# Kernel tuning notes

Hardware: AMD Instinct MI355X
Metric: run time of the kernel (lower is better)

The kernel has to match this reference:

```python
import jax, jax.numpy as jnp
import numpy as np

B, S, D, H = 2, 4096, 512, 8
HD = D // H  # 64


def setup_inputs() -> dict:
    key = jax.random.key(0)
    ks = jax.random.split(key, 9)
    def lin_init(kw, kb, fan_in, fan_out):
        bound = 1.0 / np.sqrt(fan_in)
        W = jax.random.uniform(kw, (fan_in, fan_out), minval=-bound, maxval=bound, dtype=jnp.float32)
        b = jax.random.uniform(kb, (fan_out,), minval=-bound, maxval=bound, dtype=jnp.float32)
        return W, b
    Wq, bq = lin_init(ks[0], ks[1], D, D)
    Wk, bk = lin_init(ks[2], ks[3], D, D)
    Wv, bv = lin_init(ks[4], ks[5], D, D)
    query = jax.random.normal(ks[6], (B, S, D), dtype=jnp.float32)
    key_in = jax.random.normal(ks[7], (B, S, D), dtype=jnp.float32)
    value = jax.random.normal(ks[8], (B, S, D), dtype=jnp.float32)
    return {"query": query, "key": key_in, "value": value,
            "Wq": Wq, "bq": bq, "Wk": Wk, "bk": bk, "Wv": Wv, "bv": bv}


def _split_heads(x):
    # [B, S, D] -> [B, H, S, HD]
    b, s, _ = x.shape
    return x.reshape(b, s, H, HD).transpose(0, 2, 1, 3)


def reference(query, key, value, Wq, bq, Wk, bk, Wv, bv):
    Q = _split_heads(query @ Wq + bq)
    K = _split_heads(key @ Wk + bk)
    V = _split_heads(value @ Wv + bv)
    scale = 1.0 / np.sqrt(HD).astype(np.float32)
    # scores: [B, H, Sq, Sk]
    scores = jnp.einsum('bhqd,bhkd->bhqk', Q, K) * scale
    weights = jax.nn.softmax(scores, axis=-1)
    att = jnp.einsum('bhqk,bhkd->bhqd', weights, V)
    # [B, H, S, HD] -> [B, S, D]
    return att.transpose(0, 2, 1, 3).reshape(query.shape[0], query.shape[1], D)
```

## Files before the change

### kernel.cpp

```cpp
#include <hip/hip_runtime.h>
#include <hip/hip_bf16.h>
#include <cstdint>


typedef __bf16   bf16x8 __attribute__((ext_vector_type(8)));
typedef _Float16 f16x8  __attribute__((ext_vector_type(8)));
typedef _Float16 f16x2  __attribute__((ext_vector_type(2)));
typedef float    f32x4  __attribute__((ext_vector_type(4)));
typedef float    f32x16 __attribute__((ext_vector_type(16)));
typedef unsigned int   u32;
typedef unsigned int   u32x4 __attribute__((ext_vector_type(4)));
typedef unsigned short u16;

#define NB  2
#define SEQ 4096
#define DIM 512
#define NH  8
#define HD  64
#define WSZ (DIM * DIM)
#define QSZ (NB * NH * SEQ * HD)

#if __has_builtin(__builtin_amdgcn_fdot2)
#define HAVE_FDOT2 1
#else
#define HAVE_FDOT2 0
#endif

__device__ __forceinline__ u16 f2bf(float f) {
    __bf16 h = (__bf16)f; return __builtin_bit_cast(u16, h);
}
__device__ __forceinline__ u16 f2h(float f) {
    _Float16 h = (_Float16)f; return __builtin_bit_cast(u16, h);
}
__device__ __forceinline__ u32 pack_pkrtz(float a, float b) {
    auto pk = __builtin_amdgcn_cvt_pkrtz(a, b);
    return __builtin_bit_cast(u32, pk);
}
__device__ __forceinline__ bf16x8 cvt8p(float4 a, float4 b) {
    bf16x8 o;
    o[0]=(__bf16)a.x; o[1]=(__bf16)a.y; o[2]=(__bf16)a.z; o[3]=(__bf16)a.w;
    o[4]=(__bf16)b.x; o[5]=(__bf16)b.y; o[6]=(__bf16)b.z; o[7]=(__bf16)b.w;
    return o;
}
__device__ __forceinline__ void dma16(const u16* g, u16* l) {
    __builtin_amdgcn_global_load_lds(
        (const __attribute__((address_space(1))) u32*)g,
        (__attribute__((address_space(3))) u32*)l, 16, 0, 0);
}

__global__ __launch_bounds__(256) void wt_kernel(
    const float* __restrict__ Wq, const float* __restrict__ Wk,
    const float* __restrict__ Wv, u16* __restrict__ wtImg)
{
    __shared__ u16 lT[64 * 65];
    const int p = blockIdx.z;
    const float* W = (p == 0) ? Wq : ((p == 1) ? Wk : Wv);
    const int r0 = blockIdx.x * 64, c0 = blockIdx.y * 64;
    const int t = threadIdx.x;
#pragma unroll
    for (int i = 0; i < 16; i++) {
        int idx = i * 256 + t, rowk = idx >> 6, coln = idx & 63;
        lT[coln * 65 + rowk] = f2bf(W[(size_t)(r0 + rowk) * DIM + c0 + coln]);
    }
    __syncthreads();
#pragma unroll
    for (int i = 0; i < 2; i++) {
        const int idx = i * 256 + t;
        const int nl = idx >> 3, ch = idx & 7;
        const int n = c0 + nl;
        const int row = n & 127, ntile = n >> 7;
        const int kk = (r0 >> 5) + (ch >> 2);
        const int sw = (ch & 3) ^ ((row ^ (row >> 2)) & 3);
        u16* d = wtImg + (size_t)p * WSZ + ((size_t)(ntile * 16 + kk)) * 4096
               + row * 32 + (sw << 3);
#pragma unroll
        for (int e = 0; e < 8; e++) d[e] = lT[nl * 65 + ch * 8 + e];
    }
}

__global__ __launch_bounds__(256) void proj_kernel(
    const float* __restrict__ xq, const float* __restrict__ xk,
    const float* __restrict__ xv, const u16* __restrict__ wtImg,
    const float* __restrict__ bq, const float* __restrict__ bk,
    const float* __restrict__ bv,
    u16* __restrict__ qb, u16* __restrict__ kbImg, u16* __restrict__ vtImg)
{
    __shared__ u16 smem[16384];

    const int tid = threadIdx.x;
    const int wave = tid >> 6, lane = tid & 63;
    const int l16 = lane & 15, quad = lane >> 4;
    const int wq = wave >> 1, wn = wave & 1;

    const int id = blockIdx.x;
    const int xcd = id & 7, j = id >> 3;
    const int p = j >> 5, t5 = j & 31;
    int mb, nb;
    if (p < 2) { mb = xcd * 8 + (t5 >> 2); nb = t5 & 3; }
    else       { nb = xcd * 8 + (t5 >> 2); mb = t5 & 3; }

    const float* Xp = (p == 0) ? xq : ((p == 1) ? xk : xv);
    const int xtile = (p < 2) ? mb : nb;
    const int row = tid >> 1, half = tid & 1;
    const int sr = (row ^ (row >> 2)) & 3;
    const float* xsrc = Xp + (size_t)(xtile * 128 + row) * DIM + half * 16;
    const int xldsoff = (p < 2) ? 0 : 4096;
    const int c0 = (((half * 2) ^ sr) << 3), c1 = (((half * 2 + 1) ^ sr) << 3);

    const u16* Wbase = (p < 2) ? wtImg + (size_t)p * WSZ + (size_t)nb * 16 * 4096
                               : wtImg + (size_t)2 * WSZ + (size_t)mb * 16 * 4096;
    const int wldsoff = (p < 2) ? 4096 : 0;
    const int doff = tid * 8;

    f32x4 acc[4][4];
#pragma unroll
    for (int ms = 0; ms < 4; ms++)
#pragma unroll
        for (int ns = 0; ns < 4; ns++)
#pragma unroll
            for (int jj = 0; jj < 4; jj++) acc[ms][ns][jj] = 0.f;

    {
        float4 a0 = ((const float4*)xsrc)[0], a1 = ((const float4*)xsrc)[1];
        float4 a2 = ((const float4*)xsrc)[2], a3 = ((const float4*)xsrc)[3];
        xsrc += 32;
#pragma unroll
        for (int e = 0; e < 2; e++)
            dma16(Wbase + e * 2048 + doff, smem + wldsoff + e * 2048 + doff);
        Wbase += 4096;
        u16* xd = smem + xldsoff + row * 32;
        *(bf16x8*)(xd + c0) = cvt8p(a0, a1);
        *(bf16x8*)(xd + c1) = cvt8p(a2, a3);
    }

    for (int kt = 0; kt < 16; kt++) {
        __syncthreads();
        float4 a0, a1, a2, a3;
        if (kt < 15) {
            u16* buf = smem + ((kt + 1) & 1) * 8192;
#pragma unroll
            for (int e = 0; e < 2; e++)
                dma16(Wbase + e * 2048 + doff, buf + wldsoff + e * 2048 + doff);
            Wbase += 4096;
            a0 = ((const float4*)xsrc)[0]; a1 = ((const float4*)xsrc)[1];
            a2 = ((const float4*)xsrc)[2]; a3 = ((const float4*)xsrc)[3];
            xsrc += 32;
        }
        const u16* lA = smem + (kt & 1) * 8192;
        const u16* lB = lA + 4096;

        bf16x8 af[4];
#pragma unroll
        for (int ms = 0; ms < 4; ms++) {
            const int rowa = wq * 64 + ms * 16 + l16;
            const int sra = (rowa ^ (rowa >> 2)) & 3;
            af[ms] = *(const bf16x8*)&lA[rowa * 32 + ((quad ^ sra) << 3)];
        }
#pragma unroll
        for (int ns = 0; ns < 4; ns++) {
            const int rowb = wn * 64 + ns * 16 + l16;
            const int sb = (rowb ^ (rowb >> 2)) & 3;
            const bf16x8 b = *(const bf16x8*)&lB[rowb * 32 + ((quad ^ sb) << 3)];
#pragma unroll
            for (int ms = 0; ms < 4; ms++)
                acc[ms][ns] = __builtin_amdgcn_mfma_f32_16x16x32_bf16(af[ms], b, acc[ms][ns], 0, 0, 0);
        }

        if (kt < 15) {
            u16* xd = smem + ((kt + 1) & 1) * 8192 + xldsoff + row * 32;
            *(bf16x8*)(xd + c0) = cvt8p(a0, a1);
            *(bf16x8*)(xd + c1) = cvt8p(a2, a3);
        }
    }

    __syncthreads();
    if (p < 2) {
        const float* bias = p ? bk : bq;
        const float cs = (p == 0) ? 0.18033688011112042f : 1.0f;
        const int stl = wn * 2 + wq;
        const int hh = nb * 2 + wn;
#pragma unroll
        for (int ns = 0; ns < 4; ns++) {
            const int ch = ns * 16 + l16;
            const float bval = bias[hh * 64 + ch];
#pragma unroll
            for (int ms = 0; ms < 4; ms++)
#pragma unroll
                for (int rr = 0; rr < 4; rr++) {
                    const int sqL = ms * 16 + quad * 4 + rr;
                    const float v = (acc[ms][ns][rr] + bval) * cs;
                    int off;
                    if (p == 0) off = sqL * 64 + ch;
                    else        off = sqL * 64 +
                                      (((ch >> 3) ^ ((sqL ^ (sqL >> 3)) & 7)) << 3) + (ch & 7);
                    smem[stl * 4096 + off] = f2bf(v);
                }
        }
    } else {
        const int stl = wq * 2 + wn;
#pragma unroll
        for (int ms = 0; ms < 4; ms++)
#pragma unroll
            for (int rr = 0; rr < 4; rr++) {
                const int hd = ms * 16 + quad * 4 + rr;
                const float bval = bv[mb * 128 + wq * 64 + hd];
                const int swh = (hd ^ (hd >> 3)) & 7;
#pragma unroll
                for (int ns = 0; ns < 4; ns++) {
                    const int nl = ns * 16 + l16;
                    const int sqpL = (nl & ~12) | ((nl & 8) >> 1) | ((nl & 4) << 1);
                    smem[stl * 4096 + hd * 64 +
                         (((sqpL >> 3) ^ swh) << 3) + (sqpL & 7)] =
                        f2h(acc[ms][ns][rr] + bval);
                }
            }
    }
    __syncthreads();

    {
        u16* dstp; size_t gbase;
        if (p < 2) {
            const int hh = nb * 2 + (wave >> 1);
            const int b2 = mb >> 5;
            const int row0 = (mb * 128 + (wave & 1) * 64) & 4095;
            if (p == 0) { dstp = qb;    gbase = ((size_t)(b2 * NH + hh) * 4096 + row0) * 64; }
            else        { dstp = kbImg; gbase = ((size_t)((b2 * NH + hh) * 64 + (row0 >> 6))) * 4096; }
        } else {
            const int hh = mb * 2 + (wave >> 1);
            const int b2 = nb >> 5;
            const int nblk = (nb & 31) * 2 + (wave & 1);
            dstp = vtImg; gbase = ((size_t)((b2 * NH + hh) * 64 + nblk)) * 4096;
        }
#pragma unroll
        for (int e = 0; e < 8; e++) {
            const u32x4 vv = *(const u32x4*)&smem[wave * 4096 + e * 512 + lane * 8];
            *(u32x4*)(dstp + gbase + e * 512 + lane * 8) = vv;
        }
    }
}

__global__ __launch_bounds__(512, 4) void attn_kernel(
    const u16* __restrict__ qb, const u16* __restrict__ kbImg,
    const u16* __restrict__ vtImg, float* __restrict__ out)
{
    __shared__ u16 smem[2 * 4 * 4096];
    float* cmb = (float*)smem;

    const int tid = threadIdx.x;
    const int wave = tid >> 6, lane = tid & 63;
    const int m31 = lane & 31, h = lane >> 5;
    const int wq = wave >> 1, kh = wave & 1;

    const int blk = blockIdx.x;
    const int xcd = blk & 7, idx = blk >> 3;
    const int bh = xcd * 2 + (idx >> 5);
    const int qt = idx & 31;
    const int qbase = qt * 128 + wq * 32;

    bf16x8 qF[4];
#pragma unroll
    for (int c = 0; c < 4; c++)
        qF[c] = *(const bf16x8*)(qb + ((size_t)bh * SEQ + qbase + m31) * HD + c * 16 + h * 8);

    f32x16 O0, O1;
#pragma unroll
    for (int j = 0; j < 16; j++) { O0[j] = 0.f; O1[j] = 0.f; }
    float la_ = 0.f, lb_ = 0.f;
#if HAVE_FDOT2
    const f16x2 one2 = {(_Float16)1.f, (_Float16)1.f};
#endif

    const int st  = wave >> 1;
    const int hw  = wave & 1;
    const u16* img = (st & 1) ? vtImg : kbImg;
    const u16* gp = img + ((size_t)(bh * 64 + (st >> 1) * 32)) * 4096 + hw * 2048 + lane * 8;
    {
        u16* lb = smem + st * 4096 + hw * 2048 + lane * 8;
#pragma unroll
        for (int e = 0; e < 4; e++) dma16(gp + e * 512, lb + e * 512);
        gp += 4096;
    }

    const int swV0 = (m31 ^ (m31 >> 3)) & 7;
    const int rV1  = 32 + m31;
    const int swV1 = (rV1 ^ (rV1 >> 3)) & 7;
    const int rK0  = m31;
    const int swK0 = (rK0 ^ (rK0 >> 3)) & 7;
    const int rK1  = 32 + m31;
    const int swK1 = (rK1 ^ (rK1 >> 3)) & 7;

    const int NT = 32;
    for (int it = 0; it < NT; it++) {
        __syncthreads();
        if (it + 1 < NT) {
            u16* lb = smem + ((((it + 1) & 1) * 4 + st)) * 4096 + hw * 2048 + lane * 8;
#pragma unroll
            for (int e = 0; e < 4; e++) dma16(gp + e * 512, lb + e * 512);
            gp += 4096;
        }
        const u16* sK = smem + (size_t)(((it & 1) * 4) + kh * 2) * 4096;
        const u16* sV = sK + 4096;

        bf16x8 kA0[4];
#pragma unroll
        for (int c = 0; c < 4; c++)
            kA0[c] = *(const bf16x8*)&sK[(rK0 << 6) + (((2 * c + h) ^ swK0) << 3)];

        f32x16 Sv0;
#pragma unroll
        for (int j = 0; j < 16; j++) Sv0[j] = 0.f;
        __builtin_amdgcn_s_setprio(1);
#pragma unroll
        for (int c = 0; c < 4; c++)
            Sv0 = __builtin_amdgcn_mfma_f32_32x32x16_bf16(kA0[c], qF[c], Sv0, 0, 0, 0);
        __builtin_amdgcn_s_setprio(0);

        f16x8 vA00[2], vA01[2];
#pragma unroll
        for (int c2 = 0; c2 < 2; c2++) {
            vA00[c2] = *(const f16x8*)&sV[(m31 << 6) + (((2 * c2 + h) ^ swV0) << 3)];
            vA01[c2] = *(const f16x8*)&sV[(rV1 << 6) + (((2 * c2 + h) ^ swV1) << 3)];
        }

        u32 P0[8];
#pragma unroll
        for (int mm = 0; mm < 8; mm++) {
            const float ea = __builtin_amdgcn_exp2f(Sv0[2 * mm]);
            const float eb = __builtin_amdgcn_exp2f(Sv0[2 * mm + 1]);
            P0[mm] = pack_pkrtz(ea, eb);
#if HAVE_FDOT2
            const f16x2 pp = __builtin_bit_cast(f16x2, P0[mm]);
            if (mm & 1) lb_ = __builtin_amdgcn_fdot2(pp, one2, lb_, false);
            else        la_ = __builtin_amdgcn_fdot2(pp, one2, la_, false);
#else
            if (mm & 1) lb_ += ea + eb; else la_ += ea + eb;
#endif
        }
        u32x4 g0, g1;
        g0[0] = P0[0]; g0[1] = P0[1]; g0[2] = P0[2]; g0[3] = P0[3];
        g1[0] = P0[4]; g1[1] = P0[5]; g1[2] = P0[6]; g1[3] = P0[7];
        const f16x8 pf00 = __builtin_bit_cast(f16x8, g0);
        const f16x8 pf01 = __builtin_bit_cast(f16x8, g1);

        bf16x8 kA1[4];
#pragma unroll
        for (int c = 0; c < 4; c++)
            kA1[c] = *(const bf16x8*)&sK[(rK1 << 6) + (((2 * c + h) ^ swK1) << 3)];

        f32x16 Sv1;
#pragma unroll
        for (int j = 0; j < 16; j++) Sv1[j] = 0.f;

        __builtin_amdgcn_s_setprio(1);
        Sv1 = __builtin_amdgcn_mfma_f32_32x32x16_bf16(kA1[0], qF[0], Sv1, 0, 0, 0);
        O0  = __builtin_amdgcn_mfma_f32_32x32x16_f16(vA00[0], pf00, O0, 0, 0, 0);
        Sv1 = __builtin_amdgcn_mfma_f32_32x32x16_bf16(kA1[1], qF[1], Sv1, 0, 0, 0);
        O0  = __builtin_amdgcn_mfma_f32_32x32x16_f16(vA00[1], pf01, O0, 0, 0, 0);
        Sv1 = __builtin_amdgcn_mfma_f32_32x32x16_bf16(kA1[2], qF[2], Sv1, 0, 0, 0);
        O1  = __builtin_amdgcn_mfma_f32_32x32x16_f16(vA01[0], pf00, O1, 0, 0, 0);
        Sv1 = __builtin_amdgcn_mfma_f32_32x32x16_bf16(kA1[3], qF[3], Sv1, 0, 0, 0);
        O1  = __builtin_amdgcn_mfma_f32_32x32x16_f16(vA01[1], pf01, O1, 0, 0, 0);
        __builtin_amdgcn_s_setprio(0);

        f16x8 vA10[2], vA11[2];
#pragma unroll
        for (int c2 = 0; c2 < 2; c2++) {
            vA10[c2] = *(const f16x8*)&sV[(m31 << 6) + (((4 + 2 * c2 + h) ^ swV0) << 3)];
            vA11[c2] = *(const f16x8*)&sV[(rV1 << 6) + (((4 + 2 * c2 + h) ^ swV1) << 3)];
        }

        u32 P1[8];
#pragma unroll
        for (int mm = 0; mm < 8; mm++) {
            const float ea = __builtin_amdgcn_exp2f(Sv1[2 * mm]);
            const float eb = __builtin_amdgcn_exp2f(Sv1[2 * mm + 1]);
            P1[mm] = pack_pkrtz(ea, eb);
#if HAVE_FDOT2
            const f16x2 pp = __builtin_bit_cast(f16x2, P1[mm]);
            if (mm & 1) lb_ = __builtin_amdgcn_fdot2(pp, one2, lb_, false);
            else        la_ = __builtin_amdgcn_fdot2(pp, one2, la_, false);
#else
            if (mm & 1) lb_ += ea + eb; else la_ += ea + eb;
#endif
        }
        u32x4 h0, h1;
        h0[0] = P1[0]; h0[1] = P1[1]; h0[2] = P1[2]; h0[3] = P1[3];
        h1[0] = P1[4]; h1[1] = P1[5]; h1[2] = P1[6]; h1[3] = P1[7];
        const f16x8 pf10 = __builtin_bit_cast(f16x8, h0);
        const f16x8 pf11 = __builtin_bit_cast(f16x8, h1);

        __builtin_amdgcn_s_setprio(1);
        O0 = __builtin_amdgcn_mfma_f32_32x32x16_f16(vA10[0], pf10, O0, 0, 0, 0);
        O0 = __builtin_amdgcn_mfma_f32_32x32x16_f16(vA10[1], pf11, O0, 0, 0, 0);
        O1 = __builtin_amdgcn_mfma_f32_32x32x16_f16(vA11[0], pf10, O1, 0, 0, 0);
        O1 = __builtin_amdgcn_mfma_f32_32x32x16_f16(vA11[1], pf11, O1, 0, 0, 0);
        __builtin_amdgcn_s_setprio(0);
    }

    float l_acc = la_ + lb_;
    l_acc += __shfl_xor(l_acc, 32);
    __syncthreads();
    if (kh == 1) {
#pragma unroll
        for (int hg = 0; hg < 2; hg++)
#pragma unroll
            for (int mm = 0; mm < 4; mm++) {
                f32x4 o;
#pragma unroll
                for (int j = 0; j < 4; j++) o[j] = (hg ? O1 : O0)[4 * mm + j];
                *(f32x4*)&cmb[(((wq * 2 + hg) * 4 + mm) << 8) + lane * 4] = o;
            }
        cmb[8192 + wq * 64 + lane] = l_acc;
    }
    __syncthreads();

    if (kh == 0) {
        const int b = bh >> 3, hcol = bh & 7;
        const float lt = l_acc + cmb[8192 + wq * 64 + lane];
        const float inv = 1.0f / lt;
        const int sq = qbase + m31;
#pragma unroll
        for (int hg = 0; hg < 2; hg++)
#pragma unroll
            for (int mm = 0; mm < 4; mm++) {
                const f32x4 po = *(const f32x4*)&cmb[(((wq * 2 + hg) * 4 + mm) << 8) + lane * 4];
                f32x4 o;
#pragma unroll
                for (int j = 0; j < 4; j++)
                    o[j] = ((hg ? O1 : O0)[4 * mm + j] + po[j]) * inv;
                *(f32x4*)&out[(((size_t)(b * SEQ + sq)) << 9) + hcol * 64
                              + hg * 32 + 8 * mm + 4 * h] = o;
            }
    }
}

extern "C" void kernel_launch(void* const* d_in, const int* in_sizes, int n_in,
                              void* d_out, int out_size, void* d_ws, size_t ws_size,
                              hipStream_t stream)
{
    const float* q  = (const float*)d_in[0];
    const float* k  = (const float*)d_in[1];
    const float* v  = (const float*)d_in[2];
    const float* Wq = (const float*)d_in[3];
    const float* bq = (const float*)d_in[4];
    const float* Wk = (const float*)d_in[5];
    const float* bk = (const float*)d_in[6];
    const float* Wv = (const float*)d_in[7];
    const float* bv = (const float*)d_in[8];
    float* out = (float*)d_out;

    u16* wti = (u16*)d_ws;
    u16* qbp = wti + (size_t)3 * WSZ;
    u16* kbp = qbp + (size_t)QSZ;
    u16* vtp = kbp + (size_t)QSZ;

    wt_kernel  <<<dim3(8, 8, 3), 256, 0, stream>>>(Wq, Wk, Wv, wti);
    proj_kernel<<<dim3(768),     256, 0, stream>>>(q, k, v, wti, bq, bk, bv,
                                                   qbp, kbp, vtp);
    attn_kernel<<<dim3(512),     512, 0, stream>>>(qbp, kbp, vtp, out);
}
```

Measured before the change: 205.8 us.

## Software-pipeline second score block's softmax and PV across loop iterations

Moves the exp/pack and PV MFMAs for the second 32-key sub-block into the next iteration, where they overlap with that iteration's QK MFMAs and LDS loads. A drain step after the loop finishes the last block. The V fragments for that sub-block are read from LDS before the barrier and kept in registers across it, so they stay valid. The cost is more live registers (Sv1 and vA10/vA11 carried across iterations) and the loop is forced not to unroll.

```diff
diff --git a/kernel.cpp b/kernel.cpp
--- a/kernel.cpp
+++ b/kernel.cpp
@@ -46,6 +46,32 @@
     __builtin_amdgcn_global_load_lds(
         (const __attribute__((address_space(1))) u32*)g,
         (__attribute__((address_space(3))) u32*)l, 16, 0, 0);
+}
+
+__device__ __forceinline__ void expblock(const f32x16& Sv, float& la_, float& lb_,
+                                         f16x8& pfa, f16x8& pfb) {
+#if HAVE_FDOT2
+    const f16x2 one2 = {(_Float16)1.f, (_Float16)1.f};
+#endif
+    u32 P[8];
+#pragma unroll
+    for (int mm = 0; mm < 8; mm++) {
+        const float ea = __builtin_amdgcn_exp2f(Sv[2 * mm]);
+        const float eb = __builtin_amdgcn_exp2f(Sv[2 * mm + 1]);
+        P[mm] = pack_pkrtz(ea, eb);
+#if HAVE_FDOT2
+        const f16x2 pp = __builtin_bit_cast(f16x2, P[mm]);
+        if (mm & 1) lb_ = __builtin_amdgcn_fdot2(pp, one2, lb_, false);
+        else        la_ = __builtin_amdgcn_fdot2(pp, one2, la_, false);
+#else
+        if (mm & 1) lb_ += ea + eb; else la_ += ea + eb;
+#endif
+    }
+    u32x4 w0, w1;
+    w0[0] = P[0]; w0[1] = P[1]; w0[2] = P[2]; w0[3] = P[3];
+    w1[0] = P[4]; w1[1] = P[5]; w1[2] = P[6]; w1[3] = P[7];
+    pfa = __builtin_bit_cast(f16x8, w0);
+    pfb = __builtin_bit_cast(f16x8, w1);
 }
 
 __global__ __launch_bounds__(256) void wt_kernel(
@@ -266,9 +292,6 @@
 #pragma unroll
     for (int j = 0; j < 16; j++) { O0[j] = 0.f; O1[j] = 0.f; }
     float la_ = 0.f, lb_ = 0.f;
-#if HAVE_FDOT2
-    const f16x2 one2 = {(_Float16)1.f, (_Float16)1.f};
-#endif
 
     const int st  = wave >> 1;
     const int hw  = wave & 1;
@@ -289,7 +312,13 @@
     const int rK1  = 32 + m31;
     const int swK1 = (rK1 ^ (rK1 >> 3)) & 7;
 
+    f32x16 Sv1;
+#pragma unroll
+    for (int j = 0; j < 16; j++) Sv1[j] = 0.f;
+    f16x8 vA10[2], vA11[2];
+
     const int NT = 32;
+#pragma unroll 1
     for (int it = 0; it < NT; it++) {
         __syncthreads();
         if (it + 1 < NT) {
@@ -298,6 +327,10 @@
             for (int e = 0; e < 4; e++) dma16(gp + e * 512, lb + e * 512);
             gp += 4096;
         }
+
+        f16x8 pf10, pf11;
+        if (it > 0) expblock(Sv1, la_, lb_, pf10, pf11);
+
         const u16* sK = smem + (size_t)(((it & 1) * 4) + kh * 2) * 4096;
         const u16* sV = sK + 4096;
 
@@ -305,6 +338,15 @@
 #pragma unroll
         for (int c = 0; c < 4; c++)
             kA0[c] = *(const bf16x8*)&sK[(rK0 << 6) + (((2 * c + h) ^ swK0) << 3)];
+
+        if (it > 0) {
+            __builtin_amdgcn_s_setprio(1);
+            O0 = __builtin_amdgcn_mfma_f32_32x32x16_f16(vA10[0], pf10, O0, 0, 0, 0);
+            O0 = __builtin_amdgcn_mfma_f32_32x32x16_f16(vA10[1], pf11, O0, 0, 0, 0);
+            O1 = __builtin_amdgcn_mfma_f32_32x32x16_f16(vA11[0], pf10, O1, 0, 0, 0);
+            O1 = __builtin_amdgcn_mfma_f32_32x32x16_f16(vA11[1], pf11, O1, 0, 0, 0);
+            __builtin_amdgcn_s_setprio(0);
+        }
 
         f32x16 Sv0;
 #pragma unroll
@@ -322,35 +364,16 @@
             vA01[c2] = *(const f16x8*)&sV[(rV1 << 6) + (((2 * c2 + h) ^ swV1) << 3)];
         }
 
-        u32 P0[8];
-#pragma unroll
-        for (int mm = 0; mm < 8; mm++) {
-            const float ea = __builtin_amdgcn_exp2f(Sv0[2 * mm]);
-            const float eb = __builtin_amdgcn_exp2f(Sv0[2 * mm + 1]);
-            P0[mm] = pack_pkrtz(ea, eb);
-#if HAVE_FDOT2
-            const f16x2 pp = __builtin_bit_cast(f16x2, P0[mm]);
-            if (mm & 1) lb_ = __builtin_amdgcn_fdot2(pp, one2, lb_, false);
-            else        la_ = __builtin_amdgcn_fdot2(pp, one2, la_, false);
-#else
-            if (mm & 1) lb_ += ea + eb; else la_ += ea + eb;
-#endif
-        }
-        u32x4 g0, g1;
-        g0[0] = P0[0]; g0[1] = P0[1]; g0[2] = P0[2]; g0[3] = P0[3];
-        g1[0] = P0[4]; g1[1] = P0[5]; g1[2] = P0[6]; g1[3] = P0[7];
-        const f16x8 pf00 = __builtin_bit_cast(f16x8, g0);
-        const f16x8 pf01 = __builtin_bit_cast(f16x8, g1);
-
         bf16x8 kA1[4];
 #pragma unroll
         for (int c = 0; c < 4; c++)
             kA1[c] = *(const bf16x8*)&sK[(rK1 << 6) + (((2 * c + h) ^ swK1) << 3)];
 
-        f32x16 Sv1;
+        f16x8 pf00, pf01;
+        expblock(Sv0, la_, lb_, pf00, pf01);
+
 #pragma unroll
         for (int j = 0; j < 16; j++) Sv1[j] = 0.f;
-
         __builtin_amdgcn_s_setprio(1);
         Sv1 = __builtin_amdgcn_mfma_f32_32x32x16_bf16(kA1[0], qF[0], Sv1, 0, 0, 0);
         O0  = __builtin_amdgcn_mfma_f32_32x32x16_f16(vA00[0], pf00, O0, 0, 0, 0);
@@ -362,39 +385,20 @@
         O1  = __builtin_amdgcn_mfma_f32_32x32x16_f16(vA01[1], pf01, O1, 0, 0, 0);
         __builtin_amdgcn_s_setprio(0);
 
-        f16x8 vA10[2], vA11[2];
 #pragma unroll
         for (int c2 = 0; c2 < 2; c2++) {
             vA10[c2] = *(const f16x8*)&sV[(m31 << 6) + (((4 + 2 * c2 + h) ^ swV0) << 3)];
             vA11[c2] = *(const f16x8*)&sV[(rV1 << 6) + (((4 + 2 * c2 + h) ^ swV1) << 3)];
         }
-
-        u32 P1[8];
-#pragma unroll
-        for (int mm = 0; mm < 8; mm++) {
-            const float ea = __builtin_amdgcn_exp2f(Sv1[2 * mm]);
-            const float eb = __builtin_amdgcn_exp2f(Sv1[2 * mm + 1]);
-            P1[mm] = pack_pkrtz(ea, eb);
-#if HAVE_FDOT2
-            const f16x2 pp = __builtin_bit_cast(f16x2, P1[mm]);
-            if (mm & 1) lb_ = __builtin_amdgcn_fdot2(pp, one2, lb_, false);
-            else        la_ = __builtin_amdgcn_fdot2(pp, one2, la_, false);
-#else
-            if (mm & 1) lb_ += ea + eb; else la_ += ea + eb;
-#endif
-        }
-        u32x4 h0, h1;
-        h0[0] = P1[0]; h0[1] = P1[1]; h0[2] = P1[2]; h0[3] = P1[3];
-        h1[0] = P1[4]; h1[1] = P1[5]; h1[2] = P1[6]; h1[3] = P1[7];
-        const f16x8 pf10 = __builtin_bit_cast(f16x8, h0);
-        const f16x8 pf11 = __builtin_bit_cast(f16x8, h1);
-
-        __builtin_amdgcn_s_setprio(1);
+    }
+
+    {
+        f16x8 pf10, pf11;
+        expblock(Sv1, la_, lb_, pf10, pf11);
         O0 = __builtin_amdgcn_mfma_f32_32x32x16_f16(vA10[0], pf10, O0, 0, 0, 0);
         O0 = __builtin_amdgcn_mfma_f32_32x32x16_f16(vA10[1], pf11, O0, 0, 0, 0);
         O1 = __builtin_amdgcn_mfma_f32_32x32x16_f16(vA11[0], pf10, O1, 0, 0, 0);
         O1 = __builtin_amdgcn_mfma_f32_32x32x16_f16(vA11[1], pf11, O1, 0, 0, 0);
-        __builtin_amdgcn_s_setprio(0);
     }
 
     float l_acc = la_ + lb_;
```

Result: slower. 216.9 us (+5.4%).
